# Kernel tuning notes

Measured on AMD Instinct MI355X. Metric: run time of the kernel, lower is better.

Reference implementation:

```python
import jax, jax.numpy as jnp
import numpy as np

B, D, T, G = 8, 40, 192, 256
UNITS, DEMO, OUT = 256, 16, 1


def setup_inputs() -> dict:
    key = jax.random.key(0)
    ks = jax.random.split(key, 10)
    # observation timestamps, sorted, shared across channels (per preprocessing tile)
    t1 = jnp.sort(jax.random.uniform(ks[0], (B, T)) * 48.0, axis=-1)
    times = jnp.broadcast_to(t1[:, None, :], (B, D, T))
    values = jax.random.normal(ks[1], (B, D, T))
    meas = (jax.random.uniform(ks[2], (B, D, T)) < 0.5).astype(jnp.float32)
    meas = meas.at[:, :, 0].set(1.0)  # guarantee >=1 observation per channel
    grid = jnp.broadcast_to(jnp.linspace(0.0, 48.0, G)[None, :], (B, G))
    grid_lengths = jnp.concatenate([
        jax.random.randint(ks[3], (B - 1,), G // 2, G + 1, dtype=jnp.int32),
        jnp.array([G], dtype=jnp.int32)])
    demo = jax.random.normal(ks[4], (B, DEMO))
    # learned parameters
    kernel_sic = jnp.zeros((D,))                       # softplus-param RBF widths
    cross_W = jnp.eye(D)                               # identity init
    demo_W1 = jax.random.normal(ks[5], (DEMO, UNITS)) * 0.1
    demo_b1 = jnp.zeros((UNITS,))
    demo_W2 = jax.random.normal(ks[6], (UNITS, UNITS)) * 0.05
    demo_b2 = jnp.zeros((UNITS,))
    gru_Wx = jax.random.normal(ks[7], (3 * D, 3 * UNITS)) * 0.05
    gru_Wh = jax.random.normal(ks[8], (UNITS, 3 * UNITS)) * 0.05
    gru_b = jnp.zeros((2, 3 * UNITS))                  # keras reset_after=True: [input_bias, recurrent_bias]
    out_W = jax.random.normal(ks[9], (UNITS, OUT)) * 0.1
    out_b = jnp.zeros((OUT,))
    return dict(demo=demo, times=times, values=values, measurements=meas,
                grid=grid, kernel_sic=kernel_sic, cross_W=cross_W,
                demo_W1=demo_W1, demo_b1=demo_b1, demo_W2=demo_W2, demo_b2=demo_b2,
                gru_Wx=gru_Wx, gru_Wh=gru_Wh, gru_b=gru_b,
                out_W=out_W, out_b=out_b, grid_lengths=grid_lengths)


def _forward(demo, times, values, meas, grid, kernel_sic, cross_W,
             demo_W1, demo_b1, demo_W2, demo_b2,
             gru_Wx, gru_Wh, gru_b, out_W, out_b, grid_lengths):
    # ---- single_channel_interp (reconstruction=False) ----
    logmask = jnp.where(meas > 0, 0.0, -jnp.inf)[:, :, :, None]   # [B,D,T,1]
    norm = (times[:, :, :, None] - grid[:, None, None, :]) ** 2   # [B,D,T,G]
    alpha = jax.nn.softplus(kernel_sic)[None, :, None, None]      # [1,D,1,1]

    def interp(scale):
        logits = -scale * alpha * norm + logmask                  # [B,D,T,G]
        w = jax.nn.logsumexp(logits, axis=2)                      # [B,D,G]
        p = jnp.exp(logits - w[:, :, None, :])                    # softmax over T
        y = jnp.sum(p * values[:, :, :, None], axis=2)            # [B,D,G]
        return y, w

    y, w = interp(1.0)            # smooth interpolant + log-intensity
    y_trans, _ = interp(10.0)     # sharper (transient) interpolant

    # ---- cross_channel_interp (reconstruction=False) ----
    yT = jnp.swapaxes(y, 1, 2)                                    # [B,G,D]
    wT = jnp.swapaxes(w, 1, 2)
    sw = jax.nn.softmax(wT, axis=2)                               # softmax over channels
    mean = jnp.mean(yT, axis=1, keepdims=True)                    # [B,1,D]
    rep = jnp.einsum('bgd,de->bge', sw * (yT - mean), cross_W) + mean
    rep1 = jnp.swapaxes(rep, 1, 2)                                # [B,D,G]
    intensity = jnp.exp(w)
    feats = jnp.concatenate([rep1, intensity, y_trans - rep1], axis=1)  # [B,3D,G]
    rnn_in = jnp.swapaxes(feats, 1, 2)                            # [B,G,3D]

    # ---- demo encoder -> GRU initial state ----
    h0 = jax.nn.relu(demo @ demo_W1 + demo_b1) @ demo_W2 + demo_b2

    # ---- masked GRU (keras v2, reset_after=True), return last state ----
    bi, br = gru_b[0], gru_b[1]
    Gn = rnn_in.shape[1]
    seq_mask = jnp.arange(Gn)[None, :] < grid_lengths[:, None]    # [B,G]
    x_proj = rnn_in @ gru_Wx + bi                                 # [B,G,3U]

    def step(h, inp):
        xp, m = inp                                               # [B,3U], [B]
        hp = h @ gru_Wh + br
        xz, xr, xh = jnp.split(xp, 3, axis=-1)
        hz, hr, hh = jnp.split(hp, 3, axis=-1)
        z = jax.nn.sigmoid(xz + hz)
        r = jax.nn.sigmoid(xr + hr)
        cand = jnp.tanh(xh + r * hh)
        h_new = z * h + (1.0 - z) * cand
        return jnp.where(m[:, None], h_new, h), None

    h_final, _ = jax.lax.scan(step, h0,
                              (jnp.swapaxes(x_proj, 0, 1), seq_mask.T))
    return jax.nn.sigmoid(h_final @ out_W + out_b)                # [B,OUT]


def reference(demo, times, values, measurements, grid, kernel_sic, cross_W,
              demo_W1, demo_b1, demo_W2, demo_b2,
              gru_Wx, gru_Wh, gru_b, out_W, out_b, grid_lengths):
    return _forward(demo, times, values, measurements, grid, kernel_sic, cross_W,
                    demo_W1, demo_b1, demo_W2, demo_b2,
                    gru_Wx, gru_Wh, gru_b, out_W, out_b, grid_lengths)
```

## Files before the change

kernel.cpp:

```cpp
#include <hip/hip_runtime.h>
#include <hip/hip_bf16.h>

#define B_ 8
#define D_ 40
#define T_ 192
#define G_ 256
#define U_ 768
#define H_ 256

typedef _Float16 half2_t __attribute__((ext_vector_type(2)));

__device__ inline float sigmoidf_(float x){
  return 1.0f/(1.0f+__expf(-x));
}
__device__ inline float tanhf_(float x){
  float ax = fabsf(x);
  float e = __expf(-2.0f*ax);
  float t = (1.0f-e)/(1.0f+e);
  return copysignf(t, x);
}
__device__ inline int sdot4(int a, int b, int c){
#if __has_builtin(__builtin_amdgcn_sdot4)
  return __builtin_amdgcn_sdot4(a, b, c, false);
#else
  int r = c;
  #pragma unroll
  for (int i=0;i<4;i++){
    int ai = (a << (24-8*i)) >> 24;
    int bi = (b << (24-8*i)) >> 24;
    r += ai*bi;
  }
  return r;
#endif
}
__device__ inline int pack4(int q0,int q1,int q2,int q3){
  return (q0&255) | ((q1&255)<<8) | ((q2&255)<<16) | ((q3&255)<<24);
}

__global__ __launch_bounds__(256) void k_interp(
    const float* __restrict__ times, const float* __restrict__ values,
    const float* __restrict__ meas, const float* __restrict__ grid,
    const float* __restrict__ ksic,
    float* __restrict__ y, float* __restrict__ w, float* __restrict__ ytr,
    float* __restrict__ mean){
  int bd = blockIdx.x;
  int b = bd / D_, d = bd % D_;
  int g = threadIdx.x;
  __shared__ float tt[T_], vv[T_], mm[T_];
  __shared__ float red[256];
  if (g < T_){
    tt[g] = times[bd*T_+g];
    vv[g] = values[bd*T_+g];
    mm[g] = meas[bd*T_+g];
  }
  __syncthreads();
  float alpha = log1pf(__expf(ksic[d]));
  float tg = grid[b*G_+g];
  float nmin = 3.4e38f;
  for (int t=0;t<T_;t++){
    if (mm[t] > 0.0f){
      float dd = tt[t]-tg;
      nmin = fminf(nmin, dd*dd);
    }
  }
  float s1=0.f, sv1=0.f, s10=0.f, sv10=0.f;
  for (int t=0;t<T_;t++){
    if (mm[t] > 0.0f){
      float dd = tt[t]-tg;
      float n = dd*dd - nmin;
      float e1  = __expf(-alpha*n);
      float e10 = __expf(-10.0f*alpha*n);
      s1 += e1;  sv1 += e1*vv[t];
      s10 += e10; sv10 += e10*vv[t];
    }
  }
  float yv = sv1/s1;
  float wv = -alpha*nmin + __logf(s1);
  y[bd*G_+g]   = yv;
  w[bd*G_+g]   = wv;
  ytr[bd*G_+g] = sv10/s10;
  red[g] = yv;
  __syncthreads();
  for (int s=128;s>0;s>>=1){
    if (g<s) red[g]+=red[g+s];
    __syncthreads();
  }
  if (g==0) mean[bd] = red[0]*(1.0f/(float)G_);
}

__global__ __launch_bounds__(256) void k_cross(
    const float* __restrict__ y, const float* __restrict__ w,
    const float* __restrict__ ytr, const float* __restrict__ mean,
    const float* __restrict__ crossW, const float* __restrict__ Wx,
    const float* __restrict__ gru_b, const int* __restrict__ lens,
    float* __restrict__ xproj){
  int bg = blockIdx.x;
  int b = bg >> 8, g = bg & 255;
  if (g >= lens[b]) return;
  __shared__ float wd[D_], yd[D_], ytrd[D_], md[D_], cc[D_], feats[3*D_];
  __shared__ float wstat[2];
  int tid = threadIdx.x;
  if (tid < D_){
    int idx = (b*D_+tid)*G_+g;
    wd[tid]=w[idx]; yd[tid]=y[idx]; ytrd[tid]=ytr[idx]; md[tid]=mean[b*D_+tid];
  }
  __syncthreads();
  if (tid==0){
    float mx=-3.4e38f;
    for (int d2=0;d2<D_;d2++) mx = fmaxf(mx, wd[d2]);
    float s=0.f;
    for (int d2=0;d2<D_;d2++) s += __expf(wd[d2]-mx);
    wstat[0]=mx; wstat[1]=1.0f/s;
  }
  __syncthreads();
  if (tid<D_){
    float sw = __expf(wd[tid]-wstat[0])*wstat[1];
    cc[tid] = sw*(yd[tid]-md[tid]);
  }
  __syncthreads();
  if (tid<D_){
    float acc=0.f;
    for (int d2=0;d2<D_;d2++) acc += cc[d2]*crossW[d2*D_+tid];
    float rep = acc + md[tid];
    feats[tid]       = rep;
    feats[D_+tid]    = __expf(wd[tid]);
    feats[2*D_+tid]  = ytrd[tid]-rep;
  }
  __syncthreads();
  for (int jj=0;jj<3;jj++){
    int j = tid + jj*256;
    float acc = gru_b[j];
    #pragma unroll 4
    for (int i=0;i<3*D_;i++) acc += feats[i]*Wx[i*U_+j];
    xproj[(size_t)bg*U_ + j] = acc;
  }
}

__global__ __launch_bounds__(256) void k_demo(
    const float* __restrict__ demo, const float* __restrict__ W1,
    const float* __restrict__ b1, const float* __restrict__ W2,
    const float* __restrict__ b2, float* __restrict__ h0){
  __shared__ float dl[B_*16];
  __shared__ float hid[B_*H_];
  int u = threadIdx.x;
  if (u < B_*16) dl[u] = demo[u];
  __syncthreads();
  float acc[B_];
  #pragma unroll
  for (int b=0;b<B_;b++) acc[b]=b1[u];
  for (int i=0;i<16;i++){
    float w1 = W1[i*H_+u];
    #pragma unroll
    for (int b=0;b<B_;b++) acc[b] += dl[b*16+i]*w1;
  }
  #pragma unroll
  for (int b=0;b<B_;b++) hid[b*H_+u] = fmaxf(acc[b],0.f);
  __syncthreads();
  #pragma unroll
  for (int b=0;b<B_;b++) acc[b]=b2[u];
  for (int k=0;k<H_;k++){
    float w2 = W2[k*H_+u];
    #pragma unroll
    for (int b=0;b<B_;b++) acc[b] += hid[b*H_+k]*w2;
  }
  #pragma unroll
  for (int b=0;b<B_;b++) h0[b*H_+u]=acc[b];
}

__global__ __launch_bounds__(512, 1)
void k_gru(
    const float* __restrict__ Wh, const float* __restrict__ gru_b,
    const float* __restrict__ xproj, const float* __restrict__ h0,
    const int* __restrict__ lens, const float* __restrict__ outW,
    const float* __restrict__ outb, float* __restrict__ out){
  int b = blockIdx.x;
  int t = threadIdx.x;
  int p = t >> 8;
  int j = t & 255;
  int r0 = p*128;

  __shared__ int   hq[2][64];
  __shared__ int   parti[3][H_];
  __shared__ float wmax[3][2][H_];
  __shared__ float red[H_];
  __shared__ float shs[2];

  float m0=0.f, m1=0.f, m2=0.f;
  for (int k=0;k<128;k++){
    const float* row = Wh + (size_t)(r0+k)*U_;
    m0 = fmaxf(m0, fabsf(row[j]));
    m1 = fmaxf(m1, fabsf(row[H_+j]));
    m2 = fmaxf(m2, fabsf(row[2*H_+j]));
  }
  wmax[0][p][j]=m0; wmax[1][p][j]=m1; wmax[2][p][j]=m2;

  float hj = 0.f;
  if (t < H_){
    hj = h0[b*H_+j];
    red[j] = fabsf(hj);
  }
  __syncthreads();
  for (int st=128; st>0; st>>=1){
    if (t < st) red[t] = fmaxf(red[t], red[t+st]);
    __syncthreads();
  }
  if (t==0){
    float bound = fmaxf(red[0], 1.0f);
    shs[0] = 127.0f/bound;
    shs[1] = bound/127.0f;
  }
  __syncthreads();
  float inv_sh = shs[0];
  float s_h    = shs[1];

  float cm0 = fmaxf(wmax[0][0][j], wmax[0][1][j]);
  float cm1 = fmaxf(wmax[1][0][j], wmax[1][1][j]);
  float cm2 = fmaxf(wmax[2][0][j], wmax[2][1][j]);
  float iw0 = (cm0>0.f)? 127.0f/cm0 : 0.f;
  float iw1 = (cm1>0.f)? 127.0f/cm1 : 0.f;
  float iw2 = (cm2>0.f)? 127.0f/cm2 : 0.f;
  float fz = (cm0*(1.0f/127.0f))*s_h;
  float fr = (cm1*(1.0f/127.0f))*s_h;
  float fh = (cm2*(1.0f/127.0f))*s_h;

  int wq0[32], wq1[32], wq2[32];
  #pragma unroll
  for (int k=0;k<32;k++){
    int a0,a1,a2,a3, c0,c1,c2,c3, e0,e1,e2,e3;
    {
      const float* row = Wh + (size_t)(r0+4*k+0)*U_;
      a0=(int)rintf(row[j]*iw0); c0=(int)rintf(row[H_+j]*iw1); e0=(int)rintf(row[2*H_+j]*iw2);
    }
    {
      const float* row = Wh + (size_t)(r0+4*k+1)*U_;
      a1=(int)rintf(row[j]*iw0); c1=(int)rintf(row[H_+j]*iw1); e1=(int)rintf(row[2*H_+j]*iw2);
    }
    {
      const float* row = Wh + (size_t)(r0+4*k+2)*U_;
      a2=(int)rintf(row[j]*iw0); c2=(int)rintf(row[H_+j]*iw1); e2=(int)rintf(row[2*H_+j]*iw2);
    }
    {
      const float* row = Wh + (size_t)(r0+4*k+3)*U_;
      a3=(int)rintf(row[j]*iw0); c3=(int)rintf(row[H_+j]*iw1); e3=(int)rintf(row[2*H_+j]*iw2);
    }
    wq0[k]=pack4(a0,a1,a2,a3);
    wq1[k]=pack4(c0,c1,c2,c3);
    wq2[k]=pack4(e0,e1,e2,e3);
  }

  float brz=0.f, brr=0.f, brh=0.f;
  if (p==0){
    brz = gru_b[U_+j]; brr = gru_b[U_+H_+j]; brh = gru_b[U_+2*H_+j];
    float qf = fmaxf(-127.f, fminf(127.f, rintf(hj*inv_sh)));
    ((signed char*)hq[0])[j] = (signed char)(int)qf;
  }
  int len = lens[b];
  const float* xbase = xproj + (size_t)b*G_*U_;
  float xpz=0.f, xpr=0.f, xph=0.f;
  if (p==0){
    xpz = xbase[j]; xpr = xbase[H_+j]; xph = xbase[2*H_+j];
  }
  __syncthreads();

  for (int g=0; g<len; g++){
    float nxz=0.f, nxr=0.f, nxh=0.f;
    if (p==0 && (g+1 < len)){
      const float* xn = xbase + (size_t)(g+1)*U_;
      nxz = xn[j]; nxr = xn[H_+j]; nxh = xn[2*H_+j];
    }
    const int4* hc = (const int4*)hq[g&1] + p*8;
    int az=0, ar=0, ah=0;
    #pragma unroll
    for (int c=0;c<8;c++){
      int4 hv = hc[c];
      az=sdot4(hv.x,wq0[4*c+0],az); ar=sdot4(hv.x,wq1[4*c+0],ar); ah=sdot4(hv.x,wq2[4*c+0],ah);
      az=sdot4(hv.y,wq0[4*c+1],az); ar=sdot4(hv.y,wq1[4*c+1],ar); ah=sdot4(hv.y,wq2[4*c+1],ah);
      az=sdot4(hv.z,wq0[4*c+2],az); ar=sdot4(hv.z,wq1[4*c+2],ar); ah=sdot4(hv.z,wq2[4*c+2],ah);
      az=sdot4(hv.w,wq0[4*c+3],az); ar=sdot4(hv.w,wq1[4*c+3],ar); ah=sdot4(hv.w,wq2[4*c+3],ah);
    }
    if (p){ parti[0][j]=az; parti[1][j]=ar; parti[2][j]=ah; }
    __syncthreads();
    if (p==0){
      float z    = sigmoidf_(xpz + brz + fz*(float)(az + parti[0][j]));
      float r    = sigmoidf_(xpr + brr + fr*(float)(ar + parti[1][j]));
      float cand = tanhf_(xph + r*(brh + fh*(float)(ah + parti[2][j])));
      hj = z*hj + (1.0f-z)*cand;
      float qf = fmaxf(-127.f, fminf(127.f, rintf(hj*inv_sh)));
      ((signed char*)hq[(g+1)&1])[j] = (signed char)(int)qf;
    }
    __syncthreads();
    xpz = nxz; xpr = nxr; xph = nxh;
  }

  if (t < H_) red[j] = hj*outW[j];
  __syncthreads();
  for (int st=128;st>0;st>>=1){
    if (t<st) red[t]+=red[t+st];
    __syncthreads();
  }
  if (t==0) out[b] = sigmoidf_(red[0]+outb[0]);
}

extern "C" void kernel_launch(void* const* d_in, const int* in_sizes, int n_in,
                              void* d_out, int out_size, void* d_ws, size_t ws_size,
                              hipStream_t stream) {
  const float* demo   = (const float*)d_in[0];
  const float* times  = (const float*)d_in[1];
  const float* values = (const float*)d_in[2];
  const float* meas   = (const float*)d_in[3];
  const float* grid   = (const float*)d_in[4];
  const float* ksic   = (const float*)d_in[5];
  const float* crossW = (const float*)d_in[6];
  const float* dW1    = (const float*)d_in[7];
  const float* db1    = (const float*)d_in[8];
  const float* dW2    = (const float*)d_in[9];
  const float* db2    = (const float*)d_in[10];
  const float* gWx    = (const float*)d_in[11];
  const float* gWh    = (const float*)d_in[12];
  const float* gb     = (const float*)d_in[13];
  const float* outW   = (const float*)d_in[14];
  const float* outb   = (const float*)d_in[15];
  const int*   lens   = (const int*)d_in[16];
  float* out = (float*)d_out;

  float* ws   = (float*)d_ws;
  float* y    = ws;
  float* w    = y    + B_*D_*G_;
  float* ytr  = w    + B_*D_*G_;
  float* mean = ytr  + B_*D_*G_;
  float* h0   = mean + B_*D_;
  float* xprj = h0   + B_*H_;

  k_interp<<<B_*D_, 256, 0, stream>>>(times, values, meas, grid, ksic, y, w, ytr, mean);
  k_demo  <<<1,     256, 0, stream>>>(demo, dW1, db1, dW2, db2, h0);
  k_cross <<<B_*G_, 256, 0, stream>>>(y, w, ytr, mean, crossW, gWx, gb, lens, xprj);
  k_gru   <<<B_,    512, 0, stream>>>(gWh, gb, xprj, h0, lens, outW, outb, out);
}
```

Before: 295.8 us.

## Hoist Wh int8 quantization into separate kernel and run GRU with one wave-group per batch

Moves the per-column max and int8 packing of the recurrent weights out of the GRU kernel into a new k_quant kernel that writes quantized weights to workspace, so each of the 8 GRU blocks no longer re-reads and re-quantizes the full fp32 matrix. The GRU kernel drops from 512 to 256 threads. Each thread now holds all 192 packed weight registers and does the full K=256 dot product itself, which removes the partial-sum shared-memory exchange and one barrier per timestep. This doubles per-thread serial sdot4 work and raises register pressure to about 192 VGPRs for the weights, which risks spills or lower latency hiding in the sequential recurrence.

After: 305.5 us. 1.03x slower.

```diff
diff --git a/kernel.cpp b/kernel.cpp
--- a/kernel.cpp
+++ b/kernel.cpp
@@ -7,8 +7,6 @@
 #define G_ 256
 #define U_ 768
 #define H_ 256
-
-typedef _Float16 half2_t __attribute__((ext_vector_type(2)));
 
 __device__ inline float sigmoidf_(float x){
   return 1.0f/(1.0f+__expf(-x));
@@ -167,44 +165,56 @@
   for (int b=0;b<B_;b++) h0[b*H_+u]=acc[b];
 }
 
-__global__ __launch_bounds__(512, 1)
+__global__ __launch_bounds__(256) void k_quant(
+    const float* __restrict__ Wh, int* __restrict__ wsq,
+    float* __restrict__ wmaxs){
+  int c0 = blockIdx.x*64;
+  int rg = threadIdx.x >> 6;
+  int cc = threadIdx.x & 63;
+  int col = c0 + cc;
+  float v[64];
+  float mx = 0.f;
+  #pragma unroll
+  for (int r=0;r<64;r++){
+    v[r] = Wh[(size_t)(rg*64+r)*U_ + col];
+    mx = fmaxf(mx, fabsf(v[r]));
+  }
+  __shared__ float cm[4][64];
+  cm[rg][cc] = mx;
+  __syncthreads();
+  float m = fmaxf(fmaxf(cm[0][cc],cm[1][cc]), fmaxf(cm[2][cc],cm[3][cc]));
+  float iw = (m>0.f)? 127.0f/m : 0.f;
+  if (rg==0) wmaxs[col] = m;
+  #pragma unroll
+  for (int k=0;k<16;k++){
+    int q0=(int)rintf(v[4*k+0]*iw), q1=(int)rintf(v[4*k+1]*iw),
+        q2=(int)rintf(v[4*k+2]*iw), q3=(int)rintf(v[4*k+3]*iw);
+    wsq[(size_t)(rg*16+k)*U_ + col] = pack4(q0,q1,q2,q3);
+  }
+}
+
+__global__ __launch_bounds__(256, 1)
 void k_gru(
-    const float* __restrict__ Wh, const float* __restrict__ gru_b,
+    const int* __restrict__ wsq, const float* __restrict__ wmaxs,
+    const float* __restrict__ gru_b,
     const float* __restrict__ xproj, const float* __restrict__ h0,
     const int* __restrict__ lens, const float* __restrict__ outW,
     const float* __restrict__ outb, float* __restrict__ out){
   int b = blockIdx.x;
-  int t = threadIdx.x;
-  int p = t >> 8;
-  int j = t & 255;
-  int r0 = p*128;
-
-  __shared__ int   hq[2][64];
-  __shared__ int   parti[3][H_];
-  __shared__ float wmax[3][2][H_];
+  int j = threadIdx.x;
+
+  __shared__ __align__(16) int hq[2][64];
   __shared__ float red[H_];
   __shared__ float shs[2];
 
-  float m0=0.f, m1=0.f, m2=0.f;
-  for (int k=0;k<128;k++){
-    const float* row = Wh + (size_t)(r0+k)*U_;
-    m0 = fmaxf(m0, fabsf(row[j]));
-    m1 = fmaxf(m1, fabsf(row[H_+j]));
-    m2 = fmaxf(m2, fabsf(row[2*H_+j]));
-  }
-  wmax[0][p][j]=m0; wmax[1][p][j]=m1; wmax[2][p][j]=m2;
-
-  float hj = 0.f;
-  if (t < H_){
-    hj = h0[b*H_+j];
-    red[j] = fabsf(hj);
-  }
+  float hj = h0[b*H_+j];
+  red[j] = fabsf(hj);
   __syncthreads();
   for (int st=128; st>0; st>>=1){
-    if (t < st) red[t] = fmaxf(red[t], red[t+st]);
+    if (j < st) red[j] = fmaxf(red[j], red[j+st]);
     __syncthreads();
   }
-  if (t==0){
+  if (j==0){
     float bound = fmaxf(red[0], 1.0f);
     shs[0] = 127.0f/bound;
     shs[1] = bound/127.0f;
@@ -213,92 +223,62 @@
   float inv_sh = shs[0];
   float s_h    = shs[1];
 
-  float cm0 = fmaxf(wmax[0][0][j], wmax[0][1][j]);
-  float cm1 = fmaxf(wmax[1][0][j], wmax[1][1][j]);
-  float cm2 = fmaxf(wmax[2][0][j], wmax[2][1][j]);
-  float iw0 = (cm0>0.f)? 127.0f/cm0 : 0.f;
-  float iw1 = (cm1>0.f)? 127.0f/cm1 : 0.f;
-  float iw2 = (cm2>0.f)? 127.0f/cm2 : 0.f;
+  float cm0 = wmaxs[j], cm1 = wmaxs[H_+j], cm2 = wmaxs[2*H_+j];
   float fz = (cm0*(1.0f/127.0f))*s_h;
   float fr = (cm1*(1.0f/127.0f))*s_h;
   float fh = (cm2*(1.0f/127.0f))*s_h;
-
-  int wq0[32], wq1[32], wq2[32];
-  #pragma unroll
-  for (int k=0;k<32;k++){
-    int a0,a1,a2,a3, c0,c1,c2,c3, e0,e1,e2,e3;
-    {
-      const float* row = Wh + (size_t)(r0+4*k+0)*U_;
-      a0=(int)rintf(row[j]*iw0); c0=(int)rintf(row[H_+j]*iw1); e0=(int)rintf(row[2*H_+j]*iw2);
-    }
-    {
-      const float* row = Wh + (size_t)(r0+4*k+1)*U_;
-      a1=(int)rintf(row[j]*iw0); c1=(int)rintf(row[H_+j]*iw1); e1=(int)rintf(row[2*H_+j]*iw2);
-    }
-    {
-      const float* row = Wh + (size_t)(r0+4*k+2)*U_;
-      a2=(int)rintf(row[j]*iw0); c2=(int)rintf(row[H_+j]*iw1); e2=(int)rintf(row[2*H_+j]*iw2);
-    }
-    {
-      const float* row = Wh + (size_t)(r0+4*k+3)*U_;
-      a3=(int)rintf(row[j]*iw0); c3=(int)rintf(row[H_+j]*iw1); e3=(int)rintf(row[2*H_+j]*iw2);
-    }
-    wq0[k]=pack4(a0,a1,a2,a3);
-    wq1[k]=pack4(c0,c1,c2,c3);
-    wq2[k]=pack4(e0,e1,e2,e3);
-  }
-
-  float brz=0.f, brr=0.f, brh=0.f;
-  if (p==0){
-    brz = gru_b[U_+j]; brr = gru_b[U_+H_+j]; brh = gru_b[U_+2*H_+j];
+  float brz = gru_b[U_+j], brr = gru_b[U_+H_+j], brh = gru_b[U_+2*H_+j];
+
+  int wqz[64], wqr[64], wqh[64];
+  #pragma unroll
+  for (int k=0;k<64;k++) wqz[k] = wsq[(size_t)k*U_ + j];
+  #pragma unroll
+  for (int k=0;k<64;k++) wqr[k] = wsq[(size_t)k*U_ + H_ + j];
+  #pragma unroll
+  for (int k=0;k<64;k++) wqh[k] = wsq[(size_t)k*U_ + 2*H_ + j];
+
+  {
     float qf = fmaxf(-127.f, fminf(127.f, rintf(hj*inv_sh)));
     ((signed char*)hq[0])[j] = (signed char)(int)qf;
   }
   int len = lens[b];
   const float* xbase = xproj + (size_t)b*G_*U_;
-  float xpz=0.f, xpr=0.f, xph=0.f;
-  if (p==0){
-    xpz = xbase[j]; xpr = xbase[H_+j]; xph = xbase[2*H_+j];
-  }
+  float xpz = xbase[j], xpr = xbase[H_+j], xph = xbase[2*H_+j];
   __syncthreads();
 
   for (int g=0; g<len; g++){
     float nxz=0.f, nxr=0.f, nxh=0.f;
-    if (p==0 && (g+1 < len)){
+    if (g+1 < len){
       const float* xn = xbase + (size_t)(g+1)*U_;
       nxz = xn[j]; nxr = xn[H_+j]; nxh = xn[2*H_+j];
     }
-    const int4* hc = (const int4*)hq[g&1] + p*8;
+    const int4* hc = (const int4*)hq[g&1];
     int az=0, ar=0, ah=0;
     #pragma unroll
-    for (int c=0;c<8;c++){
+    for (int c=0;c<16;c++){
       int4 hv = hc[c];
-      az=sdot4(hv.x,wq0[4*c+0],az); ar=sdot4(hv.x,wq1[4*c+0],ar); ah=sdot4(hv.x,wq2[4*c+0],ah);
-      az=sdot4(hv.y,wq0[4*c+1],az); ar=sdot4(hv.y,wq1[4*c+1],ar); ah=sdot4(hv.y,wq2[4*c+1],ah);
-      az=sdot4(hv.z,wq0[4*c+2],az); ar=sdot4(hv.z,wq1[4*c+2],ar); ah=sdot4(hv.z,wq2[4*c+2],ah);
-      az=sdot4(hv.w,wq0[4*c+3],az); ar=sdot4(hv.w,wq1[4*c+3],ar); ah=sdot4(hv.w,wq2[4*c+3],ah);
+      az=sdot4(hv.x,wqz[4*c+0],az); ar=sdot4(hv.x,wqr[4*c+0],ar); ah=sdot4(hv.x,wqh[4*c+0],ah);
+      az=sdot4(hv.y,wqz[4*c+1],az); ar=sdot4(hv.y,wqr[4*c+1],ar); ah=sdot4(hv.y,wqh[4*c+1],ah);
+      az=sdot4(hv.z,wqz[4*c+2],az); ar=sdot4(hv.z,wqr[4*c+2],ar); ah=sdot4(hv.z,wqh[4*c+2],ah);
+      az=sdot4(hv.w,wqz[4*c+3],az); ar=sdot4(hv.w,wqr[4*c+3],ar); ah=sdot4(hv.w,wqh[4*c+3],ah);
     }
-    if (p){ parti[0][j]=az; parti[1][j]=ar; parti[2][j]=ah; }
-    __syncthreads();
-    if (p==0){
-      float z    = sigmoidf_(xpz + brz + fz*(float)(az + parti[0][j]));
-      float r    = sigmoidf_(xpr + brr + fr*(float)(ar + parti[1][j]));
-      float cand = tanhf_(xph + r*(brh + fh*(float)(ah + parti[2][j])));
-      hj = z*hj + (1.0f-z)*cand;
-      float qf = fmaxf(-127.f, fminf(127.f, rintf(hj*inv_sh)));
-      ((signed char*)hq[(g+1)&1])[j] = (signed char)(int)qf;
-    }
+    float z    = sigmoidf_(xpz + brz + fz*(float)az);
+    float r    = sigmoidf_(xpr + brr + fr*(float)ar);
+    float cand = tanhf_(xph + r*(brh + fh*(float)ah));
+    hj = z*hj + (1.0f-z)*cand;
+    float qf = fmaxf(-127.f, fminf(127.f, rintf(hj*inv_sh)));
+    ((signed char*)hq[(g+1)&1])[j] = (signed char)(int)qf;
     __syncthreads();
     xpz = nxz; xpr = nxr; xph = nxh;
   }
 
-  if (t < H_) red[j] = hj*outW[j];
+  red[j] = hj*outW[j];
   __syncthreads();
   for (int st=128;st>0;st>>=1){
-    if (t<st) red[t]+=red[t+st];
+    if (j<st) red[j]+=red[j+st];
     __syncthreads();
   }
-  if (t==0) out[b] = sigmoidf_(red[0]+outb[0]);
+  if (j==0) out[b] = sigmoidf_(red[0]+outb[0]);
 }
 
 extern "C" void kernel_launch(void* const* d_in, const int* in_sizes, int n_in,
@@ -330,9 +310,12 @@
   float* mean = ytr  + B_*D_*G_;
   float* h0   = mean + B_*D_;
   float* xprj = h0   + B_*H_;
+  int*   wsq  = (int*)(xprj + (size_t)B_*G_*U_);
+  float* wmx  = (float*)(wsq + 64*U_);
 
   k_interp<<<B_*D_, 256, 0, stream>>>(times, values, meas, grid, ksic, y, w, ytr, mean);
+  k_quant <<<12,    256, 0, stream>>>(gWh, wsq, wmx);
   k_demo  <<<1,     256, 0, stream>>>(demo, dW1, db1, dW2, db2, h0);
   k_cross <<<B_*G_, 256, 0, stream>>>(y, w, ytr, mean, crossW, gWx, gb, lens, xprj);
-  k_gru   <<<B_,    512, 0, stream>>>(gWh, gb, xprj, h0, lens, outW, outb, out);
-}
+  k_gru   <<<B_,    256, 0, stream>>>(wsq, wmx, gb, xprj, h0, lens, outW, outb, out);
+}
```
